# Kernel optimization log

Hardware: AMD Instinct MI355X
Metric: run time of the kernel (lower is better)

## Reference

```python
import jax, jax.numpy as jnp
import numpy as np

B, S, D, H = 4, 2048, 1024, 1024

def setup_inputs() -> dict:
    key = jax.random.key(0)
    ks = jax.random.split(key, 9)
    s_in = 1.0 / np.sqrt(D)
    s_h = 1.0 / np.sqrt(H)
    return {
        "x": jax.random.normal(ks[0], (B, S, D), dtype=jnp.float32),
        "Wq": jax.random.normal(ks[1], (D, H), dtype=jnp.float32) * s_in,
        "bq": jnp.zeros((H,), dtype=jnp.float32),
        "Wk": jax.random.normal(ks[2], (D, H), dtype=jnp.float32) * s_in,
        "bk": jnp.zeros((H,), dtype=jnp.float32),
        "Wv": jax.random.normal(ks[3], (D, H), dtype=jnp.float32) * s_in,
        "bv": jnp.zeros((H,), dtype=jnp.float32),
        "Wo": jax.random.normal(ks[4], (H, D), dtype=jnp.float32) * s_h,
        "bo": jnp.zeros((D,), dtype=jnp.float32),
    }

def reference(x, Wq, bq, Wk, bk, Wv, bv, Wo, bo):
    # q,k,v: [B,S,H]
    q = jnp.einsum("bsd,dh->bsh", x, Wq) + bq
    k = jnp.einsum("bsd,dh->bsh", x, Wk) + bk
    v = jnp.einsum("bsd,dh->bsh", x, Wv) + bv
    # NOTE: original module has NO 1/sqrt(d) scaling
    scores = jnp.einsum("bqh,bkh->bqk", q, k)  # [B,S,S]
    attn = jax.nn.softmax(scores, axis=-1)
    y = jnp.einsum("bqk,bkh->bqh", attn, v)
    return jnp.einsum("bsh,hd->bsd", y, Wo) + bo
```

## Files before the change

kernel.cpp:

```cpp
#include <hip/hip_runtime.h>

typedef _Float16 f16x8 __attribute__((ext_vector_type(8)));
typedef float f32x4 __attribute__((ext_vector_type(4)));

#define GLD16(gp, lp) __builtin_amdgcn_global_load_lds(                     \
    (const __attribute__((address_space(1))) void*)(gp),                    \
    (__attribute__((address_space(3))) void*)(lp), 16, 0, 0)

__device__ inline void xcd_swizzle(int& bx, int& by) {
    const int nwg = gridDim.x * gridDim.y;
    const int flat = blockIdx.y * gridDim.x + blockIdx.x;
    const int cpx = nwg >> 3;
    const int swz = (flat & 7) * cpx + (flat >> 3);
    bx = swz % gridDim.x;
    by = swz / gridDim.x;
}

template <int MODE, int BN>
__global__ __launch_bounds__(256)
void gemm_nt(const _Float16* __restrict__ A, const _Float16* __restrict__ B,
             void* __restrict__ C, const float* __restrict__ bias,
             int K, int lda, int ldb, int ldc, size_t sA, size_t sB, size_t sC)
{
    constexpr int NJ = BN / 32;
    __shared__ __align__(16) _Float16 lA[128 * 32];
    __shared__ __align__(16) _Float16 lB[BN * 32];
    const int tid = threadIdx.x, wave = tid >> 6, lane = tid & 63;
    const int z = blockIdx.z;
    int bx, by; xcd_swizzle(bx, by);
    const _Float16* Ab = A + (size_t)z * sA;
    const _Float16* Bb = B + (size_t)z * sB;
    const int m0 = by * 128, n0 = bx * BN;
    const int wr = (wave >> 1) * 64, wc = (wave & 1) * (BN / 2);
    const int srow = wave * 16 + (lane >> 2);
    const int scb  = (((lane & 3) ^ ((srow >> 1) & 3))) * 16;

    const char* gA = (const char*)(Ab + (size_t)(m0 + srow) * lda) + scb;
    const char* gB = (const char*)(Bb + (size_t)(n0 + srow) * ldb) + scb;
    const size_t rstepA = (size_t)64 * lda * 2;
    const size_t rstepB = (size_t)64 * ldb * 2;
    char* lAb = (char*)lA + wave * 1024;
    char* lBb = (char*)lB + wave * 1024;

    const int fr = lane & 15;
    const int ckq = ((lane >> 4) ^ ((fr >> 1) & 3)) * 8;
    const _Float16* rA = lA + (wr + fr) * 32 + ckq;
    const _Float16* rB = lB + (wc + fr) * 32 + ckq;

    const f32x4 zero = {0.f, 0.f, 0.f, 0.f};
    f32x4 acc[4][NJ];
#pragma unroll
    for (int i = 0; i < 4; ++i)
#pragma unroll
        for (int j = 0; j < NJ; ++j) acc[i][j] = zero;

    for (int k0 = 0; k0 < K; k0 += 32) {
        GLD16(gA, lAb); GLD16(gA + rstepA, lAb + 4096);
        GLD16(gB, lBb);
        if constexpr (BN == 128) GLD16(gB + rstepB, lBb + 4096);
        gA += 64; gB += 64;
        __syncthreads();
        f16x8 af[4], bf[NJ];
#pragma unroll
        for (int i = 0; i < 4; ++i) af[i] = *(const f16x8*)(rA + i * 512);
#pragma unroll
        for (int j = 0; j < NJ; ++j) bf[j] = *(const f16x8*)(rB + j * 512);
#pragma unroll
        for (int i = 0; i < 4; ++i)
#pragma unroll
            for (int j = 0; j < NJ; ++j)
                acc[i][j] = __builtin_amdgcn_mfma_f32_16x16x32_f16(
                    af[i], bf[j], acc[i][j], 0, 0, 0);
        __syncthreads();
    }

    const int r0 = (lane >> 4) * 4;
#pragma unroll
    for (int j = 0; j < NJ; ++j) {
        const int col = n0 + wc + j * 16 + fr;
        const float bv = bias ? bias[col] : 0.0f;
#pragma unroll
        for (int i = 0; i < 4; ++i) {
            const int row = m0 + wr + i * 16 + r0;
            if constexpr (MODE == 0) {
                float* p = (float*)C + (size_t)z * sC + (size_t)row * ldc + col;
                p[0]               = acc[i][j][0] + bv;
                p[(size_t)ldc]     = acc[i][j][1] + bv;
                p[(size_t)2 * ldc] = acc[i][j][2] + bv;
                p[(size_t)3 * ldc] = acc[i][j][3] + bv;
            } else if constexpr (MODE == 1) {
                _Float16* p = (_Float16*)C + (size_t)z * sC + (size_t)row * ldc + col;
                p[0]               = (_Float16)(acc[i][j][0] + bv);
                p[(size_t)ldc]     = (_Float16)(acc[i][j][1] + bv);
                p[(size_t)2 * ldc] = (_Float16)(acc[i][j][2] + bv);
                p[(size_t)3 * ldc] = (_Float16)(acc[i][j][3] + bv);
            } else {
                const int bb = row >> 11, s = row & 2047;
                _Float16* p = (_Float16*)C + (((size_t)(bb << 10) + col) << 11) + s;
                p[0] = (_Float16)(acc[i][j][0] + bv);
                p[1] = (_Float16)(acc[i][j][1] + bv);
                p[2] = (_Float16)(acc[i][j][2] + bv);
                p[3] = (_Float16)(acc[i][j][3] + bv);
            }
        }
    }
}

template <int MODE>
__global__ __launch_bounds__(512, 2)
void gemm_spa256(const _Float16* __restrict__ Ah, const _Float16* __restrict__ Al,
                 const _Float16* __restrict__ B,
                 void* __restrict__ Cm, _Float16* __restrict__ Ca,
                 const float* __restrict__ bias,
                 int K, int lda, int ldb, int ldc, int CaCols,
                 size_t sA, size_t sB, size_t sC)
{
    __shared__ __align__(16) _Float16 lds[2][3][256 * 32];
    const int tid = threadIdx.x, wave = tid >> 6, lane = tid & 63;
    const int z = blockIdx.z;
    int bx, by; xcd_swizzle(bx, by);
    const int m0 = by * 256, n0 = bx * 256;

    const int trow = tid >> 2;
    const int schunk = (tid & 3) ^ ((trow >> 1) & 3);
    const char* pAh = (const char*)(Ah + (size_t)z * sA + (size_t)(m0 + trow) * lda) + schunk * 16;
    const char* pAl = (const char*)(Al + (size_t)z * sA + (size_t)(m0 + trow) * lda) + schunk * 16;
    const char* pB  = (const char*)(B  + (size_t)z * sB + (size_t)(n0 + trow) * ldb) + schunk * 16;
    const size_t hA = (size_t)128 * lda * 2;
    const size_t hB = (size_t)128 * ldb * 2;

    auto stage = [&](int bf) {
        char* d0 = (char*)&lds[bf][0][0] + tid * 16;
        char* d1 = (char*)&lds[bf][1][0] + tid * 16;
        char* d2 = (char*)&lds[bf][2][0] + tid * 16;
        GLD16(pAh, d0); GLD16(pAh + hA, d0 + 8192);
        GLD16(pAl, d1); GLD16(pAl + hA, d1 + 8192);
        GLD16(pB,  d2); GLD16(pB  + hB, d2 + 8192);
        pAh += 64; pAl += 64; pB += 64;
    };

    const int wr = (wave >> 1) * 64, wcol = (wave & 1) * 128;
    const int fr = lane & 15;
    const int ckq = ((lane >> 4) ^ ((fr >> 1) & 3)) * 8;
    const int nt = K >> 5;

    const f32x4 zero = {0.f, 0.f, 0.f, 0.f};
    f32x4 acc[4][8];
#pragma unroll
    for (int i = 0; i < 4; ++i)
#pragma unroll
        for (int j = 0; j < 8; ++j) acc[i][j] = zero;

    stage(0); stage(1);
    asm volatile("s_waitcnt vmcnt(6)" ::: "memory");
    __builtin_amdgcn_s_barrier();
    __builtin_amdgcn_sched_barrier(0);

    for (int t = 0; t < nt; ++t) {
        const int cur = t & 1;
        const _Float16* bAh = &lds[cur][0][0];
        const _Float16* bAl = &lds[cur][1][0];
        const _Float16* bB  = &lds[cur][2][0];
        f16x8 af[4], al4[4], bf8[8];
#pragma unroll
        for (int i = 0; i < 4; ++i) {
            af[i]  = *(const f16x8*)(bAh + (wr + i * 16 + fr) * 32 + ckq);
            al4[i] = *(const f16x8*)(bAl + (wr + i * 16 + fr) * 32 + ckq);
        }
#pragma unroll
        for (int j = 0; j < 8; ++j)
            bf8[j] = *(const f16x8*)(bB + (wcol + j * 16 + fr) * 32 + ckq);
        __builtin_amdgcn_sched_barrier(0);
        __builtin_amdgcn_s_barrier();
        if (t + 2 < nt) stage(cur);
        __builtin_amdgcn_s_setprio(1);
#pragma unroll
        for (int i = 0; i < 4; ++i)
#pragma unroll
            for (int j = 0; j < 8; ++j) {
                acc[i][j] = __builtin_amdgcn_mfma_f32_16x16x32_f16(af[i],  bf8[j], acc[i][j], 0, 0, 0);
                acc[i][j] = __builtin_amdgcn_mfma_f32_16x16x32_f16(al4[i], bf8[j], acc[i][j], 0, 0, 0);
            }
        __builtin_amdgcn_s_setprio(0);
        __builtin_amdgcn_sched_barrier(0);
        if (t + 2 < nt) { asm volatile("s_waitcnt vmcnt(6)" ::: "memory"); }
        else           { asm volatile("s_waitcnt vmcnt(0)" ::: "memory"); }
        __builtin_amdgcn_s_barrier();
        __builtin_amdgcn_sched_barrier(0);
    }

    const int r0 = (lane >> 4) * 4;
#pragma unroll
    for (int j = 0; j < 8; ++j) {
        const int col = n0 + wcol + j * 16 + fr;
        const float bv = (MODE == 1 && bias) ? bias[col] : 0.0f;
#pragma unroll
        for (int i = 0; i < 4; ++i) {
            const int row = m0 + wr + i * 16 + r0;
#pragma unroll
            for (int r = 0; r < 4; ++r) {
                const float val = acc[i][j][r] + bv;
                const size_t idx = (size_t)z * sC + (size_t)(row + r) * ldc + col;
                if constexpr (MODE == 0) {
                    ((float*)Cm)[idx] = val;
                } else {
                    const _Float16 hv = (_Float16)val;
                    ((_Float16*)Cm)[idx] = hv;
                    if (col < CaCols) Ca[idx] = (_Float16)(val - (float)hv);
                }
            }
        }
    }
}

template <int MODE>
__global__ __launch_bounds__(512, 2)
void gemm_nt256(const _Float16* __restrict__ A, const _Float16* __restrict__ B,
                void* __restrict__ Cm, _Float16* __restrict__ Ca,
                const float* __restrict__ bias,
                int K, int lda, int ldb, int ldc, int CaCols,
                size_t sA, size_t sB, size_t sC)
{
    __shared__ __align__(16) _Float16 lds[2][2][256 * 32];
    const int tid = threadIdx.x, wave = tid >> 6, lane = tid & 63;
    const int z = blockIdx.z;
    int bx, by; xcd_swizzle(bx, by);
    const int m0 = by * 256, n0 = bx * 256;

    const int trow = tid >> 2;
    const int schunk = (tid & 3) ^ ((trow >> 1) & 3);
    const char* pA = (const char*)(A + (size_t)z * sA + (size_t)(m0 + trow) * lda) + schunk * 16;
    const char* pB = (const char*)(B + (size_t)z * sB + (size_t)(n0 + trow) * ldb) + schunk * 16;
    const size_t hA = (size_t)128 * lda * 2;
    const size_t hB = (size_t)128 * ldb * 2;

    auto stage = [&](int bf) {
        char* d0 = (char*)&lds[bf][0][0] + tid * 16;
        char* d1 = (char*)&lds[bf][1][0] + tid * 16;
        GLD16(pA, d0); GLD16(pA + hA, d0 + 8192);
        GLD16(pB, d1); GLD16(pB + hB, d1 + 8192);
        pA += 64; pB += 64;
    };

    const int wr = (wave >> 1) * 64, wcol = (wave & 1) * 128;
    const int fr = lane & 15;
    const int ckq = ((lane >> 4) ^ ((fr >> 1) & 3)) * 8;
    const int nt = K >> 5;

    const f32x4 zero = {0.f, 0.f, 0.f, 0.f};
    f32x4 acc[4][8];
#pragma unroll
    for (int i = 0; i < 4; ++i)
#pragma unroll
        for (int j = 0; j < 8; ++j) acc[i][j] = zero;

    stage(0); stage(1);
    asm volatile("s_waitcnt vmcnt(4)" ::: "memory");
    __builtin_amdgcn_s_barrier();
    __builtin_amdgcn_sched_barrier(0);

    for (int t = 0; t < nt; ++t) {
        const int cur = t & 1;
        const _Float16* bA = &lds[cur][0][0];
        const _Float16* bB = &lds[cur][1][0];
        f16x8 af[4], bf8[8];
#pragma unroll
        for (int i = 0; i < 4; ++i)
            af[i] = *(const f16x8*)(bA + (wr + i * 16 + fr) * 32 + ckq);
#pragma unroll
        for (int j = 0; j < 8; ++j)
            bf8[j] = *(const f16x8*)(bB + (wcol + j * 16 + fr) * 32 + ckq);
        __builtin_amdgcn_sched_barrier(0);
        __builtin_amdgcn_s_barrier();
        if (t + 2 < nt) stage(cur);
        __builtin_amdgcn_s_setprio(1);
#pragma unroll
        for (int i = 0; i < 4; ++i)
#pragma unroll
            for (int j = 0; j < 8; ++j)
                acc[i][j] = __builtin_amdgcn_mfma_f32_16x16x32_f16(af[i], bf8[j], acc[i][j], 0, 0, 0);
        __builtin_amdgcn_s_setprio(0);
        __builtin_amdgcn_sched_barrier(0);
        if (t + 2 < nt) { asm volatile("s_waitcnt vmcnt(4)" ::: "memory"); }
        else           { asm volatile("s_waitcnt vmcnt(0)" ::: "memory"); }
        __builtin_amdgcn_s_barrier();
        __builtin_amdgcn_sched_barrier(0);
    }

    const int r0 = (lane >> 4) * 4;
#pragma unroll
    for (int j = 0; j < 8; ++j) {
        const int col = n0 + wcol + j * 16 + fr;
        const float bv = bias ? bias[col] : 0.0f;
#pragma unroll
        for (int i = 0; i < 4; ++i) {
            const int row = m0 + wr + i * 16 + r0;
#pragma unroll
            for (int r = 0; r < 4; ++r) {
                const float val = acc[i][j][r] + bv;
                const size_t idx = (size_t)z * sC + (size_t)(row + r) * ldc + col;
                const _Float16 hv = (_Float16)val;
                ((_Float16*)Cm)[idx] = hv;
                if (col < CaCols) Ca[idx] = (_Float16)(val - (float)hv);
            }
        }
    }
}

__global__ __launch_bounds__(256)
void cvt_split_f16(const float* __restrict__ in, _Float16* __restrict__ hi,
                   _Float16* __restrict__ lo, int n8)
{
    const int t = blockIdx.x * 256 + threadIdx.x;
    if (t >= n8) return;
    const float4* p = (const float4*)in + (size_t)t * 2;
    const float4 a = p[0], b = p[1];
    const float v[8] = {a.x, a.y, a.z, a.w, b.x, b.y, b.z, b.w};
    f16x8 h, l;
#pragma unroll
    for (int j = 0; j < 8; ++j) {
        const _Float16 hv = (_Float16)v[j];
        h[j] = hv;
        l[j] = (_Float16)(v[j] - (float)hv);
    }
    ((f16x8*)hi)[t] = h;
    if (lo) ((f16x8*)lo)[t] = l;
}

__global__ __launch_bounds__(256)
void transpose_f16(const float* __restrict__ W, _Float16* __restrict__ hiT,
                   int rows, int cols)
{
    __shared__ float t[32][33];
    const int c0 = blockIdx.x * 32, r0 = blockIdx.y * 32;
    const int tx = threadIdx.x & 31, ty = threadIdx.x >> 5;
#pragma unroll
    for (int r = ty; r < 32; r += 8)
        t[r][tx] = W[(size_t)(r0 + r) * cols + (c0 + tx)];
    __syncthreads();
#pragma unroll
    for (int r = ty; r < 32; r += 8)
        hiT[(size_t)(c0 + r) * rows + (r0 + tx)] = (_Float16)t[tx][r];
}

__global__ __launch_bounds__(256)
void concat_bias(const float* __restrict__ a, const float* __restrict__ b,
                 float* __restrict__ o)
{
    const int t = blockIdx.x * 256 + threadIdx.x;
    o[t] = (t < 1024) ? a[t] : b[t - 1024];
}

__global__ __launch_bounds__(256)
void softmax_rows(const float* __restrict__ S, _Float16* __restrict__ P)
{
    const int row = blockIdx.x;
    const float* s = S + (size_t)row * 2048 + threadIdx.x * 8;
    float v[8];
    const float4 a = *(const float4*)s;
    const float4 b = *(const float4*)(s + 4);
    v[0] = a.x; v[1] = a.y; v[2] = a.z; v[3] = a.w;
    v[4] = b.x; v[5] = b.y; v[6] = b.z; v[7] = b.w;
    float mx = v[0];
#pragma unroll
    for (int j = 1; j < 8; ++j) mx = fmaxf(mx, v[j]);
    for (int off = 32; off; off >>= 1) mx = fmaxf(mx, __shfl_xor(mx, off, 64));
    __shared__ float redm[4], reds[4];
    const int wv = threadIdx.x >> 6;
    if ((threadIdx.x & 63) == 0) redm[wv] = mx;
    __syncthreads();
    mx = fmaxf(fmaxf(redm[0], redm[1]), fmaxf(redm[2], redm[3]));
    float sum = 0.f;
#pragma unroll
    for (int j = 0; j < 8; ++j) { v[j] = expf(v[j] - mx); sum += v[j]; }
    for (int off = 32; off; off >>= 1) sum += __shfl_xor(sum, off, 64);
    if ((threadIdx.x & 63) == 0) reds[wv] = sum;
    __syncthreads();
    const float inv = 1.0f / (reds[0] + reds[1] + reds[2] + reds[3]);
    f16x8 o;
#pragma unroll
    for (int j = 0; j < 8; ++j) o[j] = (_Float16)(v[j] * inv);
    *(f16x8*)(P + (size_t)row * 2048 + threadIdx.x * 8) = o;
}

extern "C" void kernel_launch(void* const* d_in, const int* in_sizes, int n_in,
                              void* d_out, int out_size, void* d_ws, size_t ws_size,
                              hipStream_t stream)
{
    (void)in_sizes; (void)n_in; (void)out_size;
    const float* x  = (const float*)d_in[0];
    const float* Wq = (const float*)d_in[1];
    const float* bq = (const float*)d_in[2];
    const float* Wk = (const float*)d_in[3];
    const float* bk = (const float*)d_in[4];
    const float* Wv = (const float*)d_in[5];
    const float* bv = (const float*)d_in[6];
    const float* Wo = (const float*)d_in[7];
    const float* bo = (const float*)d_in[8];
    float* out = (float*)d_out;

    constexpr int S = 2048, D = 1024, H = 1024, NBATCH = 4;
    constexpr size_t M  = (size_t)NBATCH * S;
    constexpr size_t SH = (size_t)S * H;
    constexpr size_t SS = (size_t)S * S;
    constexpr size_t QK = (size_t)S * 2048;

    char* w = (char*)d_ws;
    size_t off = 0;
    auto alloc = [&](size_t bytes) -> char* {
        char* p = w + off;
        off += (bytes + 255) & ~(size_t)255;
        return p;
    };

    _Float16* xh   = (_Float16*)alloc(M * D * 2);
    _Float16* wqkT = (_Float16*)alloc((size_t)2 * D * H * 2);
    _Float16* wvh  = (_Float16*)alloc((size_t)D * H * 2);
    _Float16* woh  = (_Float16*)alloc((size_t)H * D * 2);
    float*    bqk  = (float*)alloc(2048 * 4);
    _Float16* qkh  = (_Float16*)alloc(M * 2048 * 2);
    _Float16* qkl  = (_Float16*)alloc(M * 2048 * 2);
    _Float16* vT   = (_Float16*)alloc(M * H * 2);
    _Float16* yh   = xh;

    int NB = 1;
    if (ws_size >= off + (size_t)4 * SS * 4 + (size_t)4 * SS * 2 + 1024) NB = 4;
    float*    sc = (float*)alloc((size_t)NB * SS * 4);
    _Float16* Ph = (_Float16*)alloc((size_t)NB * SS * 2);

    cvt_split_f16<<<dim3((unsigned)(M * D / 8 / 256)), 256, 0, stream>>>(
        x, xh, nullptr, (int)(M * D / 8));
    dim3 tg(H / 32, D / 32);
    transpose_f16<<<tg, 256, 0, stream>>>(Wq, wqkT, D, H);
    transpose_f16<<<tg, 256, 0, stream>>>(Wk, wqkT + (size_t)D * H, D, H);
    transpose_f16<<<tg, 256, 0, stream>>>(Wv, wvh, D, H);
    transpose_f16<<<tg, 256, 0, stream>>>(Wo, woh, H, D);
    concat_bias<<<dim3(8), 256, 0, stream>>>(bq, bk, bqk);

    gemm_nt256<1><<<dim3(2048 / 256, M / 256), 512, 0, stream>>>(
        xh, wqkT, qkh, qkl, bqk,
        D, D, D, 2048, 1024, 0, 0, 0);

    gemm_nt<2, 64><<<dim3(H / 64, M / 128), 256, 0, stream>>>(
        xh, wvh, vT, bv, D, D, D, 0, 0, 0, 0);

    for (int b0 = 0; b0 < NBATCH; b0 += NB) {
        gemm_spa256<0><<<dim3(S / 256, S / 256, NB), 512, 0, stream>>>(
            qkh + (size_t)b0 * QK, qkl + (size_t)b0 * QK,
            qkh + (size_t)b0 * QK + 1024,
            sc, nullptr, nullptr,
            H, 2048, 2048, S, 0, QK, QK, SS);
        softmax_rows<<<dim3(NB * S), 256, 0, stream>>>(sc, Ph);
        gemm_nt<1, 64><<<dim3(H / 64, S / 128, NB), 256, 0, stream>>>(
            Ph, vT + (size_t)b0 * SH, yh + (size_t)b0 * SH, nullptr,
            S, S, S, H, SS, SH, SH);
    }

    gemm_nt<0, 64><<<dim3(D / 64, M / 128), 256, 0, stream>>>(
        yh, woh, out, bo, H, H, H, D, 0, 0, 0);
}
```

Baseline: 282.1 us.

## Replace gemm_nt with double-buffered 128x256 pipelined GEMM for V, PV and output projections

Replaces the single-buffered 128x64 GEMM kernel with a 512-thread 128x256 tile kernel. It double-buffers LDS and issues async global-to-LDS loads two stages ahead, using explicit vmcnt waits, barriers and setprio around the MFMA block. The aim is to hide memory latency behind compute and to raise operand reuse per tile for the V projection, the attention-times-V GEMM and the output projection. The larger tile produces fewer workgroups (e.g. 4x64 for the V projection) and uses more LDS per block, which can cost occupancy and load balance across CUs.

```diff
diff --git a/kernel.cpp b/kernel.cpp
--- a/kernel.cpp
+++ b/kernel.cpp
@@ -16,68 +16,81 @@
     by = swz / gridDim.x;
 }
 
-template <int MODE, int BN>
-__global__ __launch_bounds__(256)
-void gemm_nt(const _Float16* __restrict__ A, const _Float16* __restrict__ B,
+template <int MODE>
+__global__ __launch_bounds__(512, 2)
+void gemm_pl(const _Float16* __restrict__ A, const _Float16* __restrict__ B,
              void* __restrict__ C, const float* __restrict__ bias,
              int K, int lda, int ldb, int ldc, size_t sA, size_t sB, size_t sC)
 {
-    constexpr int NJ = BN / 32;
-    __shared__ __align__(16) _Float16 lA[128 * 32];
-    __shared__ __align__(16) _Float16 lB[BN * 32];
+    __shared__ __align__(16) _Float16 lds[2][(128 + 256) * 32];
     const int tid = threadIdx.x, wave = tid >> 6, lane = tid & 63;
     const int z = blockIdx.z;
     int bx, by; xcd_swizzle(bx, by);
-    const _Float16* Ab = A + (size_t)z * sA;
-    const _Float16* Bb = B + (size_t)z * sB;
-    const int m0 = by * 128, n0 = bx * BN;
-    const int wr = (wave >> 1) * 64, wc = (wave & 1) * (BN / 2);
-    const int srow = wave * 16 + (lane >> 2);
-    const int scb  = (((lane & 3) ^ ((srow >> 1) & 3))) * 16;
-
-    const char* gA = (const char*)(Ab + (size_t)(m0 + srow) * lda) + scb;
-    const char* gB = (const char*)(Bb + (size_t)(n0 + srow) * ldb) + scb;
-    const size_t rstepA = (size_t)64 * lda * 2;
-    const size_t rstepB = (size_t)64 * ldb * 2;
-    char* lAb = (char*)lA + wave * 1024;
-    char* lBb = (char*)lB + wave * 1024;
-
+    const int m0 = by * 128, n0 = bx * 256;
+
+    const int trow = tid >> 2;
+    const int schunk = (tid & 3) ^ ((trow >> 1) & 3);
+    const char* pA = (const char*)(A + (size_t)z * sA + (size_t)(m0 + trow) * lda) + schunk * 16;
+    const char* pB = (const char*)(B + (size_t)z * sB + (size_t)(n0 + trow) * ldb) + schunk * 16;
+    const size_t hB = (size_t)128 * ldb * 2;
+
+    auto stage = [&](int bf) {
+        char* dA = (char*)&lds[bf][0] + tid * 16;
+        char* dB = (char*)&lds[bf][128 * 32] + tid * 16;
+        GLD16(pA, dA);
+        GLD16(pB, dB); GLD16(pB + hB, dB + 8192);
+        pA += 64; pB += 64;
+    };
+
+    const int wr = (wave >> 2) * 64, wcol = (wave & 3) * 64;
     const int fr = lane & 15;
     const int ckq = ((lane >> 4) ^ ((fr >> 1) & 3)) * 8;
-    const _Float16* rA = lA + (wr + fr) * 32 + ckq;
-    const _Float16* rB = lB + (wc + fr) * 32 + ckq;
+    const int nt = K >> 5;
 
     const f32x4 zero = {0.f, 0.f, 0.f, 0.f};
-    f32x4 acc[4][NJ];
+    f32x4 acc[4][4];
 #pragma unroll
     for (int i = 0; i < 4; ++i)
 #pragma unroll
-        for (int j = 0; j < NJ; ++j) acc[i][j] = zero;
-
-    for (int k0 = 0; k0 < K; k0 += 32) {
-        GLD16(gA, lAb); GLD16(gA + rstepA, lAb + 4096);
-        GLD16(gB, lBb);
-        if constexpr (BN == 128) GLD16(gB + rstepB, lBb + 4096);
-        gA += 64; gB += 64;
-        __syncthreads();
-        f16x8 af[4], bf[NJ];
-#pragma unroll
-        for (int i = 0; i < 4; ++i) af[i] = *(const f16x8*)(rA + i * 512);
-#pragma unroll
-        for (int j = 0; j < NJ; ++j) bf[j] = *(const f16x8*)(rB + j * 512);
+        for (int j = 0; j < 4; ++j) acc[i][j] = zero;
+
+    stage(0); stage(1);
+    asm volatile("s_waitcnt vmcnt(3)" ::: "memory");
+    __builtin_amdgcn_s_barrier();
+    __builtin_amdgcn_sched_barrier(0);
+
+    for (int t = 0; t < nt; ++t) {
+        const int cur = t & 1;
+        const _Float16* bA = &lds[cur][0];
+        const _Float16* bB = &lds[cur][128 * 32];
+        f16x8 af[4], bf4[4];
 #pragma unroll
         for (int i = 0; i < 4; ++i)
-#pragma unroll
-            for (int j = 0; j < NJ; ++j)
-                acc[i][j] = __builtin_amdgcn_mfma_f32_16x16x32_f16(
-                    af[i], bf[j], acc[i][j], 0, 0, 0);
-        __syncthreads();
+            af[i] = *(const f16x8*)(bA + (wr + i * 16 + fr) * 32 + ckq);
+#pragma unroll
+        for (int j = 0; j < 4; ++j)
+            bf4[j] = *(const f16x8*)(bB + (wcol + j * 16 + fr) * 32 + ckq);
+        __builtin_amdgcn_sched_barrier(0);
+        __builtin_amdgcn_s_barrier();
+        if (t + 2 < nt) stage(cur);
+        __builtin_amdgcn_s_setprio(1);
+#pragma unroll
+        for (int i = 0; i < 4; ++i)
+#pragma unroll
+            for (int j = 0; j < 4; ++j)
+                acc[i][j] = __builtin_amdgcn_mfma_f32_16x16x32_f16(af[i], bf4[j], acc[i][j], 0, 0, 0);
+        __builtin_amdgcn_s_setprio(0);
+        __builtin_amdgcn_sched_barrier(0);
+        if (t + 2 < nt) { asm volatile("s_waitcnt vmcnt(3)" ::: "memory"); }
+        else           { asm volatile("s_waitcnt vmcnt(0)" ::: "memory"); }
+        __builtin_amdgcn_s_barrier();
+        __builtin_amdgcn_sched_barrier(0);
     }
 
     const int r0 = (lane >> 4) * 4;
 #pragma unroll
-    for (int j = 0; j < NJ; ++j) {
-        const int col = n0 + wc + j * 16 + fr;
+    for (int j = 0; j < 4; ++j) {
+        const int col = n0 + wcol + j * 16 + fr;
         const float bv = bias ? bias[col] : 0.0f;
 #pragma unroll
         for (int i = 0; i < 4; ++i) {
@@ -441,7 +454,7 @@
         xh, wqkT, qkh, qkl, bqk,
         D, D, D, 2048, 1024, 0, 0, 0);
 
-    gemm_nt<2, 64><<<dim3(H / 64, M / 128), 256, 0, stream>>>(
+    gemm_pl<2><<<dim3(H / 256, M / 128), 512, 0, stream>>>(
         xh, wvh, vT, bv, D, D, D, 0, 0, 0, 0);
 
     for (int b0 = 0; b0 < NBATCH; b0 += NB) {
@@ -451,11 +464,11 @@
             sc, nullptr, nullptr,
             H, 2048, 2048, S, 0, QK, QK, SS);
         softmax_rows<<<dim3(NB * S), 256, 0, stream>>>(sc, Ph);
-        gemm_nt<1, 64><<<dim3(H / 64, S / 128, NB), 256, 0, stream>>>(
+        gemm_pl<1><<<dim3(H / 256, S / 128, NB), 512, 0, stream>>>(
             Ph, vT + (size_t)b0 * SH, yh + (size_t)b0 * SH, nullptr,
             S, S, S, H, SS, SH, SH);
     }
 
-    gemm_nt<0, 64><<<dim3(D / 64, M / 128), 256, 0, stream>>>(
+    gemm_pl<0><<<dim3(D / 256, M / 128), 512, 0, stream>>>(
         yh, woh, out, bo, H, H, H, D, 0, 0, 0);
 }
```

Result: faster. 255.3 us (-9.5%).
